# Optimization experiments

Measured on AMD Instinct MI355X. Metric: run time of the kernel, lower is better.

## Reference

```python
import jax, jax.numpy as jnp
import numpy as np

EPS_IN = 1e-5   # InstanceNorm2d default eps
EPS_VAR = 1e-6  # clamp on attention variance

def instance_norm(x):
    # x: (b, c, h, w); affine=False, biased variance over spatial dims
    mean = jnp.mean(x, axis=(2, 3), keepdims=True)
    var = jnp.var(x, axis=(2, 3), keepdims=True)
    return (x - mean) * jax.lax.rsqrt(var + EPS_IN)

def setup_inputs() -> dict:
    key = jax.random.key(0)
    k1, k2, k3, k4 = jax.random.split(key, 4)
    shp = (4, 512, 64, 64)
    return {
        "c_x": jax.random.normal(k1, shp, dtype=jnp.float32),
        "s_x": jax.random.normal(k2, shp, dtype=jnp.float32),
        "c_1x": jax.random.normal(k3, shp, dtype=jnp.float32),
        "s_1x": jax.random.normal(k4, shp, dtype=jnp.float32),
    }

def reference(c_x, s_x, c_1x, s_1x):
    b, v_dim, h, w = c_x.shape
    hw = h * w
    # Q: (b, hw, qk), K: (b, qk, hw), V: (b, hw, v)
    Q = instance_norm(c_1x).reshape(b, -1, hw).transpose(0, 2, 1)
    K = instance_norm(s_1x).reshape(b, -1, s_1x.shape[2] * s_1x.shape[3])
    V = s_x.reshape(b, v_dim, -1).transpose(0, 2, 1)
    # attention over spatial tokens
    A = jax.nn.softmax(jnp.einsum('bqc,bck->bqk', Q, K), axis=-1)
    M = jnp.einsum('bqk,bkv->bqv', A, V)              # weighted mean
    Var = jnp.einsum('bqk,bkv->bqv', A, V * V) - M * M  # weighted variance
    S = jnp.sqrt(jnp.clip(Var, EPS_VAR, None))
    # back to (b, v, h, w)
    M = M.reshape(b, h, w, -1).transpose(0, 3, 1, 2)
    S = S.reshape(b, h, w, -1).transpose(0, 3, 1, 2)
    return S * instance_norm(c_x) + M
```

## Files before the change

### kernel.cpp

```cpp
#include <hip/hip_runtime.h>
#include <cmath>


#define B_  4
#define C_  512
#define HW_ 4096

typedef _Float16 f16;
typedef _Float16 f16x8 __attribute__((ext_vector_type(8)));
typedef float    f32x4 __attribute__((ext_vector_type(4)));

__device__ __forceinline__ f32x4 mfma16(f16x8 a, f16x8 b, f32x4 c) {
  return __builtin_amdgcn_mfma_f32_16x16x32_f16(a, b, c, 0, 0, 0);
}
__device__ __forceinline__ void g2l16(const f16* g, f16* l) {
  __builtin_amdgcn_global_load_lds(
      (const __attribute__((address_space(1))) void*)g,
      (__attribute__((address_space(3))) void*)l, 16, 0, 0);
}

__global__ __launch_bounds__(256) void k_stats(
    const float* __restrict__ cx, const float* __restrict__ c1,
    const float* __restrict__ s1,
    float2* __restrict__ cxs, float2* __restrict__ c1s, float2* __restrict__ s1s) {
  int c = blockIdx.x, b = blockIdx.y, t = blockIdx.z;
  const float* src = (t == 0 ? cx : (t == 1 ? c1 : s1)) + (size_t)(b * C_ + c) * HW_;
  float s = 0.f, q = 0.f;
  const float4* src4 = (const float4*)src;
  for (int i = threadIdx.x; i < HW_ / 4; i += 256) {
    float4 v = src4[i];
    s += v.x + v.y + v.z + v.w;
    q += v.x * v.x + v.y * v.y + v.z * v.z + v.w * v.w;
  }
#pragma unroll
  for (int off = 1; off < 64; off <<= 1) {
    s += __shfl_xor(s, off);
    q += __shfl_xor(q, off);
  }
  __shared__ float ss[4], sq[4];
  int wv = threadIdx.x >> 6;
  if ((threadIdx.x & 63) == 0) { ss[wv] = s; sq[wv] = q; }
  __syncthreads();
  if (threadIdx.x == 0) {
    float S = ss[0] + ss[1] + ss[2] + ss[3];
    float Q = sq[0] + sq[1] + sq[2] + sq[3];
    float mean = S * (1.f / HW_);
    float var = Q * (1.f / HW_) - mean * mean;
    float2 r;
    r.x = mean;
    r.y = rsqrtf(var + 1e-5f);
    (t == 0 ? cxs : (t == 1 ? c1s : s1s))[b * C_ + c] = r;
  }
}

__global__ __launch_bounds__(256) void k_prept(
    const float* __restrict__ src, const float2* __restrict__ st,
    f16* __restrict__ dst) {
  int pb = blockIdx.x * 64, cb = blockIdx.y * 64, b = blockIdx.z;
  __shared__ float t[64][65];
  int tj = threadIdx.x & 63, tr = threadIdx.x >> 6;
#pragma unroll 4
  for (int p = 0; p < 16; ++p) {
    int cl = p * 4 + tr;
    float2 mr = st[b * C_ + cb + cl];
    float v = src[(size_t)(b * C_ + cb + cl) * HW_ + pb + tj];
    t[cl][tj] = (v - mr.x) * mr.y;
  }
  __syncthreads();
#pragma unroll 4
  for (int p = 0; p < 16; ++p) {
    int pr = p * 4 + tr;
    dst[(size_t)(b * HW_ + pb + pr) * C_ + cb + tj] = (f16)t[tj][pr];
  }
}

__global__ __launch_bounds__(256) void k_prepv(const float* __restrict__ src,
                                               f16* __restrict__ dst) {
  int gid = blockIdx.x * 256 + threadIdx.x;
  const float4* s = (const float4*)src + (size_t)gid * 2;
  float4 v0 = s[0], v1 = s[1];
  f16x8 v = {(f16)v0.x, (f16)v0.y, (f16)v0.z, (f16)v0.w,
             (f16)v1.x, (f16)v1.y, (f16)v1.z, (f16)v1.w};
  *(f16x8*)(dst + (size_t)gid * 8) = v;
}

__global__ __launch_bounds__(512, 2) void k_qk(
    const f16* __restrict__ Qt, const f16* __restrict__ Kt,
    f16* __restrict__ E, float2* __restrict__ mlpart,
    int qspan, int qt256, int npair) {
  int id = blockIdx.x, pair, kt;
  if ((npair & 7) == 0) {
    int xcd = id & 7, j = id >> 3, qrs = npair >> 3;
    pair = xcd * qrs + (j % qrs);
    kt = j / qrs;
  } else {
    pair = id >> 4;
    kt = id & 15;
  }
  int bz = pair / qt256, qt = pair - bz * qt256;

  const f16* Aq = Qt + ((size_t)(bz * qspan + qt * 256)) * C_;
  const f16* Bk = Kt + (size_t)bz * HW_ * C_ + (size_t)kt * 256 * C_;
  f16* Eb = E + ((size_t)(bz * qspan + qt * 256)) * HW_ + kt * 256;
  float2* mlb = mlpart + ((size_t)(bz * qspan + qt * 256)) * 16 + kt;

  __shared__ __align__(16) union ShQK {
    f16 ring[2 * 32768];
    f16 ebuf[64 * 272];
  } sh;
  __shared__ float sred[2][256];

  int t = threadIdx.x, wave = t >> 6, lane = t & 63, lq = lane & 15, quad = lane >> 4;
  int wy = wave >> 1, wx = wave & 1;

  int srow = t >> 3;
  int scol = ((t & 7) ^ (srow & 7)) * 8;

  int aoff = (wy * 64 + lq) * 64;
  int boff = 16384 + (wx * 128 + lq) * 64;
  int cx0 = (quad * 8) ^ ((lq & 7) << 3);
  int cx1 = (32 + quad * 8) ^ ((lq & 7) << 3);

  f32x4 acc[4][8];
#pragma unroll
  for (int mt = 0; mt < 4; ++mt)
#pragma unroll
    for (int nt = 0; nt < 8; ++nt) acc[mt][nt] = (f32x4){0, 0, 0, 0};

#pragma unroll
  for (int i = 0; i < 4; ++i)
    g2l16(Aq + (size_t)(i * 64 + srow) * C_ + scol, sh.ring + i * 4096 + t * 8);
#pragma unroll
  for (int i = 0; i < 4; ++i)
    g2l16(Bk + (size_t)(i * 64 + srow) * C_ + scol, sh.ring + 16384 + i * 4096 + t * 8);
  asm volatile("s_waitcnt vmcnt(0)" ::: "memory");
  __builtin_amdgcn_s_barrier();

  int cur = 0;
  for (int s = 0; s < 8; ++s) {
    const f16* base = sh.ring + cur * 32768;
    int nxOff = (cur ^ 1) * 32768;
    bool st = s < 7;
    int c1g = (s + 1) * 64;

    f16x8 af[4], bf[8];
#pragma unroll
    for (int mt = 0; mt < 4; ++mt)
      af[mt] = *(const f16x8*)(base + aoff + mt * 1024 + cx0);
#pragma unroll
    for (int nt = 0; nt < 8; ++nt)
      bf[nt] = *(const f16x8*)(base + boff + nt * 1024 + cx0);
    if (st) {
#pragma unroll
      for (int i = 0; i < 4; ++i)
        g2l16(Aq + (size_t)(i * 64 + srow) * C_ + c1g + scol,
              sh.ring + nxOff + i * 4096 + t * 8);
    }
    asm volatile("s_waitcnt lgkmcnt(0)" ::: "memory");
    __builtin_amdgcn_sched_barrier(0);
    __builtin_amdgcn_s_setprio(1);
#pragma unroll
    for (int mt = 0; mt < 4; ++mt)
#pragma unroll
      for (int nt = 0; nt < 8; ++nt)
        acc[mt][nt] = mfma16(af[mt], bf[nt], acc[mt][nt]);
    __builtin_amdgcn_s_setprio(0);

#pragma unroll
    for (int mt = 0; mt < 4; ++mt)
      af[mt] = *(const f16x8*)(base + aoff + mt * 1024 + cx1);
#pragma unroll
    for (int nt = 0; nt < 8; ++nt)
      bf[nt] = *(const f16x8*)(base + boff + nt * 1024 + cx1);
    if (st) {
#pragma unroll
      for (int i = 0; i < 4; ++i)
        g2l16(Bk + (size_t)(i * 64 + srow) * C_ + c1g + scol,
              sh.ring + nxOff + 16384 + i * 4096 + t * 8);
    }
    asm volatile("s_waitcnt lgkmcnt(0)" ::: "memory");
    __builtin_amdgcn_sched_barrier(0);
    __builtin_amdgcn_s_setprio(1);
#pragma unroll
    for (int mt = 0; mt < 4; ++mt)
#pragma unroll
      for (int nt = 0; nt < 8; ++nt)
        acc[mt][nt] = mfma16(af[mt], bf[nt], acc[mt][nt]);
    __builtin_amdgcn_s_setprio(0);

    asm volatile("s_waitcnt vmcnt(0)" ::: "memory");
    __builtin_amdgcn_s_barrier();
    cur ^= 1;
  }

#pragma unroll
  for (int mt = 0; mt < 4; ++mt)
#pragma unroll
    for (int r = 0; r < 4; ++r) {
      float v = -1e30f;
#pragma unroll
      for (int nt = 0; nt < 8; ++nt) v = fmaxf(v, acc[mt][nt][r]);
#pragma unroll
      for (int msk = 1; msk < 16; msk <<= 1) v = fmaxf(v, __shfl_xor(v, msk));
      if (lq == 0) sred[wx][wy * 64 + mt * 16 + quad * 4 + r] = v;
    }
  __syncthreads();
  float mrow[4][4];
#pragma unroll
  for (int mt = 0; mt < 4; ++mt)
#pragma unroll
    for (int r = 0; r < 4; ++r) {
      int rr = wy * 64 + mt * 16 + quad * 4 + r;
      mrow[mt][r] = fmaxf(sred[0][rr], sred[1][rr]);
    }

  float rsum[4][4];
#pragma unroll
  for (int mt = 0; mt < 4; ++mt)
#pragma unroll
    for (int r = 0; r < 4; ++r) rsum[mt][r] = 0.f;

#pragma unroll
  for (int mt = 0; mt < 4; ++mt) {
    __syncthreads();
#pragma unroll
    for (int nt = 0; nt < 8; ++nt) {
      f32x4 v = acc[mt][nt];
      int cs = ((wx * 16 + nt * 2 + (lq >> 3)) ^ (quad << 1)) * 8 + (lq & 7);
#pragma unroll
      for (int r = 0; r < 4; ++r) {
        float e = __expf(v[r] - mrow[mt][r]);
        rsum[mt][r] += e;
        sh.ebuf[(wy * 16 + quad * 4 + r) * 272 + cs] = (f16)e;
      }
    }
    __syncthreads();
#pragma unroll
    for (int i = 0; i < 4; ++i) {
      int idx = i * 512 + t;
      int rl = idx >> 5, ck = idx & 31;
      int cr = (ck ^ (((rl >> 2) & 3) << 1)) * 8;
      f16x8 v8 = *(const f16x8*)(sh.ebuf + rl * 272 + cr);
      int grow = (rl >> 4) * 64 + mt * 16 + (rl & 15);
      *(f16x8*)(Eb + (size_t)grow * HW_ + ck * 8) = v8;
    }
  }

#pragma unroll
  for (int mt = 0; mt < 4; ++mt)
#pragma unroll
    for (int r = 0; r < 4; ++r) {
      float v = rsum[mt][r];
#pragma unroll
      for (int msk = 1; msk < 16; msk <<= 1) v += __shfl_xor(v, msk);
      if (lq == 0) sred[wx][wy * 64 + mt * 16 + quad * 4 + r] = v;
    }
  __syncthreads();
  if (wx == 0 && lq == 0) {
#pragma unroll
    for (int mt = 0; mt < 4; ++mt)
#pragma unroll
      for (int r = 0; r < 4; ++r) {
        int rr = wy * 64 + mt * 16 + quad * 4 + r;
        mlb[(size_t)rr * 16] = make_float2(mrow[mt][r], sred[0][rr] + sred[1][rr]);
      }
  }
}

__global__ __launch_bounds__(256) void k_red(const float2* __restrict__ mlpart,
                                             float* __restrict__ alpha) {
  int row = blockIdx.x * 256 + threadIdx.x;
  const float2* p = mlpart + (size_t)row * 16;
  float2 loc[16];
  float m = -1e30f;
#pragma unroll
  for (int i = 0; i < 16; ++i) {
    loc[i] = p[i];
    m = fmaxf(m, loc[i].x);
  }
  float l = 0.f;
#pragma unroll
  for (int i = 0; i < 16; ++i) l += loc[i].y * __expf(loc[i].x - m);
  float invl = 1.f / l;
#pragma unroll
  for (int i = 0; i < 16; ++i)
    alpha[(size_t)row * 16 + i] = __expf(loc[i].x - m) * invl;
}

#define PV_STAGE_A(i)                                                         \
  g2l16(Ap + (size_t)((i)*64 + srow) * HW_ + s2 * 64 + scol,                  \
        sm + pnOff + (i)*4096 + t * 8)
#define PV_STAGE_B(i)                                                         \
  g2l16(Bv + (size_t)((i)*64 + srow) * HW_ + s2 * 64 + scol,                  \
        sm + pnOff + 16384 + (i)*4096 + t * 8)

#define PV_PHASE(CX, STAGE_STMT, POST_STMT)                                   \
  {                                                                           \
    f16x8 af0 = *(const f16x8*)(As_s + aoff + 0 * 1024 + (CX));               \
    f16x8 af1 = *(const f16x8*)(As_s + aoff + 1 * 1024 + (CX));               \
    f16x8 af2 = *(const f16x8*)(As_s + aoff + 2 * 1024 + (CX));               \
    f16x8 af3 = *(const f16x8*)(As_s + aoff + 3 * 1024 + (CX));               \
    f16x8 bf0 = *(const f16x8*)(Bs_s + boff + 0 * 1024 + (CX));               \
    f16x8 bf1 = *(const f16x8*)(Bs_s + boff + 1 * 1024 + (CX));               \
    f16x8 bf2 = *(const f16x8*)(Bs_s + boff + 2 * 1024 + (CX));               \
    f16x8 bf3 = *(const f16x8*)(Bs_s + boff + 3 * 1024 + (CX));               \
    STAGE_STMT;                                                               \
    asm volatile("s_waitcnt lgkmcnt(0)" ::: "memory");                        \
    __builtin_amdgcn_sched_barrier(0);                                        \
    __builtin_amdgcn_s_setprio(1);                                            \
    af0 *= aal[0]; af1 *= aal[1]; af2 *= aal[2]; af3 *= aal[3];               \
    f16x8 q0 = bf0 * bf0, q1 = bf1 * bf1, q2 = bf2 * bf2, q3 = bf3 * bf3;     \
    accM [0][0] = mfma16(af0, bf0, accM [0][0]);                              \
    accM2[0][0] = mfma16(af0, q0,  accM2[0][0]);                              \
    accM [0][1] = mfma16(af0, bf1, accM [0][1]);                              \
    accM2[0][1] = mfma16(af0, q1,  accM2[0][1]);                              \
    accM [0][2] = mfma16(af0, bf2, accM [0][2]);                              \
    accM2[0][2] = mfma16(af0, q2,  accM2[0][2]);                              \
    accM [0][3] = mfma16(af0, bf3, accM [0][3]);                              \
    accM2[0][3] = mfma16(af0, q3,  accM2[0][3]);                              \
    accM [1][0] = mfma16(af1, bf0, accM [1][0]);                              \
    accM2[1][0] = mfma16(af1, q0,  accM2[1][0]);                              \
    accM [1][1] = mfma16(af1, bf1, accM [1][1]);                              \
    accM2[1][1] = mfma16(af1, q1,  accM2[1][1]);                              \
    accM [1][2] = mfma16(af1, bf2, accM [1][2]);                              \
    accM2[1][2] = mfma16(af1, q2,  accM2[1][2]);                              \
    accM [1][3] = mfma16(af1, bf3, accM [1][3]);                              \
    accM2[1][3] = mfma16(af1, q3,  accM2[1][3]);                              \
    accM [2][0] = mfma16(af2, bf0, accM [2][0]);                              \
    accM2[2][0] = mfma16(af2, q0,  accM2[2][0]);                              \
    accM [2][1] = mfma16(af2, bf1, accM [2][1]);                              \
    accM2[2][1] = mfma16(af2, q1,  accM2[2][1]);                              \
    accM [2][2] = mfma16(af2, bf2, accM [2][2]);                              \
    accM2[2][2] = mfma16(af2, q2,  accM2[2][2]);                              \
    accM [2][3] = mfma16(af2, bf3, accM [2][3]);                              \
    accM2[2][3] = mfma16(af2, q3,  accM2[2][3]);                              \
    accM [3][0] = mfma16(af3, bf0, accM [3][0]);                              \
    accM2[3][0] = mfma16(af3, q0,  accM2[3][0]);                              \
    accM [3][1] = mfma16(af3, bf1, accM [3][1]);                              \
    accM2[3][1] = mfma16(af3, q1,  accM2[3][1]);                              \
    accM [3][2] = mfma16(af3, bf2, accM [3][2]);                              \
    accM2[3][2] = mfma16(af3, q2,  accM2[3][2]);                              \
    accM [3][3] = mfma16(af3, bf3, accM [3][3]);                              \
    accM2[3][3] = mfma16(af3, q3,  accM2[3][3]);                              \
    __builtin_amdgcn_s_setprio(0);                                            \
    POST_STMT;                                                                \
  }

__global__ __launch_bounds__(512, 2) void k_pv(
    const f16* __restrict__ P, const float* __restrict__ alphaG,
    const f16* __restrict__ V, const float* __restrict__ cx,
    const float2* __restrict__ cxs, float* __restrict__ out,
    int qspan, int qbase, int qt256) {
  int npairs = (int)gridDim.x >> 2;
  int id = blockIdx.x, pair, ct;
  if ((npairs & 7) == 0) {
    int x = id & 7, j = id >> 3, ppx = npairs >> 3;
    pair = x * ppx + (j >> 2);
    ct = j & 3;
  } else {
    pair = id >> 2;
    ct = id & 3;
  }
  int bz = pair / qt256, qt = pair - bz * qt256;

  const f16* Ap = P + ((size_t)(bz * qspan + qt * 256)) * HW_;
  const f16* Bv = V + ((size_t)(bz * C_ + ct * 128)) * HW_;

  __shared__ __align__(16) f16 sm[3 * 24576 + 256 * 17];
  f16* Alh = sm + 3 * 24576;

  int t = threadIdx.x, wave = t >> 6, lane = t & 63, lq = lane & 15, quad = lane >> 4;
  int wy = wave >> 1, wx = wave & 1;

  {
    const float* ag = alphaG + ((size_t)(bz * qspan + qt * 256)) * 16;
#pragma unroll
    for (int i = 0; i < 8; ++i) {
      int e = i * 512 + t;
      Alh[(e >> 4) * 17 + (e & 15)] = (f16)ag[e];
    }
  }

  int srow = t >> 3;
  int scol = ((t & 7) ^ (srow & 7)) * 8;

  int aoff = (wy * 64 + lq) * 64;
  int boff = (wx * 64 + lq) * 64;
  int cx0 = (quad * 8) ^ ((lq & 7) << 3);
  int cx1 = (32 + quad * 8) ^ ((lq & 7) << 3);

  f32x4 accM[4][4], accM2[4][4];
#pragma unroll
  for (int mt = 0; mt < 4; ++mt)
#pragma unroll
    for (int nt = 0; nt < 4; ++nt) {
      accM[mt][nt] = (f32x4){0, 0, 0, 0};
      accM2[mt][nt] = (f32x4){0, 0, 0, 0};
    }

#pragma unroll
  for (int s0 = 0; s0 < 2; ++s0) {
    int off = s0 * 24576;
#pragma unroll
    for (int i = 0; i < 4; ++i)
      g2l16(Ap + (size_t)(i * 64 + srow) * HW_ + s0 * 64 + scol,
            sm + off + i * 4096 + t * 8);
#pragma unroll
    for (int i = 0; i < 2; ++i)
      g2l16(Bv + (size_t)(i * 64 + srow) * HW_ + s0 * 64 + scol,
            sm + off + 16384 + i * 4096 + t * 8);
  }
  asm volatile("s_waitcnt lgkmcnt(0)" ::: "memory");
  asm volatile("s_waitcnt vmcnt(6)" ::: "memory");
  __builtin_amdgcn_s_barrier();

  int ph = 0, pn = 2;
  for (int s = 0; s < 64; ++s) {
    const f16* As_s = sm + ph * 24576;
    const f16* Bs_s = As_s + 16384;
    int pnOff = pn * 24576;
    int s2 = s + 2;
    bool st = s < 62;
    int ktl = s >> 2;
    f16 aal[4];
    aal[0] = Alh[(wy * 64 + lq +  0) * 17 + ktl];
    aal[1] = Alh[(wy * 64 + lq + 16) * 17 + ktl];
    aal[2] = Alh[(wy * 64 + lq + 32) * 17 + ktl];
    aal[3] = Alh[(wy * 64 + lq + 48) * 17 + ktl];

    PV_PHASE(cx0,
             if (st) { PV_STAGE_A(0); PV_STAGE_A(1); PV_STAGE_A(2); }, )
    PV_PHASE(cx1,
             if (st) { PV_STAGE_A(3); PV_STAGE_B(0); PV_STAGE_B(1); },
             if (st) { asm volatile("s_waitcnt vmcnt(6)" ::: "memory"); }
             else    { asm volatile("s_waitcnt vmcnt(0)" ::: "memory"); })
    __builtin_amdgcn_s_barrier();

    ph = (ph == 2) ? 0 : ph + 1;
    pn = (pn == 2) ? 0 : pn + 1;
  }

  int chbase = ct * 128 + wx * 64;
#pragma unroll
  for (int mt = 0; mt < 4; ++mt) {
    int q0 = qbase + qt * 256 + wy * 64 + mt * 16 + quad * 4;
#pragma unroll
    for (int nt = 0; nt < 4; ++nt) {
      int c = chbase + nt * 16 + lq;
      float2 stc = cxs[bz * C_ + c];
      size_t base = ((size_t)bz * C_ + c) * HW_ + q0;
      float4 cv = *(const float4*)(cx + base);
      f32x4 m1 = accM[mt][nt], m2 = accM2[mt][nt];
      float4 o;
      o.x = sqrtf(fmaxf(m2[0] - m1[0] * m1[0], 1e-6f)) * ((cv.x - stc.x) * stc.y) + m1[0];
      o.y = sqrtf(fmaxf(m2[1] - m1[1] * m1[1], 1e-6f)) * ((cv.y - stc.x) * stc.y) + m1[1];
      o.z = sqrtf(fmaxf(m2[2] - m1[2] * m1[2], 1e-6f)) * ((cv.z - stc.x) * stc.y) + m1[2];
      o.w = sqrtf(fmaxf(m2[3] - m1[3] * m1[3], 1e-6f)) * ((cv.w - stc.x) * stc.y) + m1[3];
      *(float4*)(out + base) = o;
    }
  }
}

extern "C" void kernel_launch(void* const* d_in, const int* in_sizes, int n_in,
                              void* d_out, int out_size, void* d_ws,
                              size_t ws_size, hipStream_t stream) {
  const float* c_x = (const float*)d_in[0];
  const float* s_x = (const float*)d_in[1];
  const float* c1x = (const float*)d_in[2];
  const float* s1x = (const float*)d_in[3];
  float* out = (float*)d_out;

  char* ws = (char*)d_ws;
  size_t o = 0;
  f16* Qt = (f16*)(ws + o);  o += (size_t)B_ * HW_ * C_ * 2;
  f16* Kt = (f16*)(ws + o);  o += (size_t)B_ * HW_ * C_ * 2;
  f16* Vh = (f16*)(ws + o);  o += (size_t)B_ * HW_ * C_ * 2;
  float2* cxs = (float2*)(ws + o); o += B_ * C_ * sizeof(float2);
  float2* c1s = (float2*)(ws + o); o += B_ * C_ * sizeof(float2);
  float2* s1s = (float2*)(ws + o); o += B_ * C_ * sizeof(float2);
  size_t fixed = (o + 255) & ~(size_t)255;

  const size_t per_row = (size_t)HW_ * 2 + 16 * 8 + 16 * 4;
  struct Cfg { int nb, qs; };
  const Cfg cfgs[5] = {{4, 4096}, {1, 4096}, {1, 2048}, {1, 1024}, {1, 512}};
  Cfg cfg = cfgs[4];
  for (int i = 0; i < 5; ++i) {
    size_t rows = (size_t)cfgs[i].nb * cfgs[i].qs;
    if (fixed + rows * per_row <= ws_size) { cfg = cfgs[i]; break; }
  }
  const int nb = cfg.nb, qspan = cfg.qs, qt256 = qspan / 256;
  const int npair256 = nb * qt256;
  const size_t rows = (size_t)nb * qspan;
  f16* E = (f16*)(ws + fixed);
  float2* mlpart = (float2*)(ws + fixed + rows * HW_ * 2);
  float* alpha = (float*)(ws + fixed + rows * HW_ * 2 + rows * 16 * 8);

  k_stats<<<dim3(C_, B_, 3), 256, 0, stream>>>(c_x, c1x, s1x, cxs, c1s, s1s);
  k_prept<<<dim3(HW_ / 64, C_ / 64, B_), 256, 0, stream>>>(c1x, c1s, Qt);
  k_prept<<<dim3(HW_ / 64, C_ / 64, B_), 256, 0, stream>>>(s1x, s1s, Kt);
  k_prepv<<<dim3(B_ * C_ * HW_ / 8 / 256), 256, 0, stream>>>(s_x, Vh);

  for (int b0 = 0; b0 < B_; b0 += nb) {
    for (int qb = 0; qb < HW_; qb += qspan) {
      const f16* Qtp = Qt + ((size_t)b0 * HW_ + qb) * C_;
      const f16* Ktp = Kt + (size_t)b0 * HW_ * C_;
      const f16* Vp = Vh + (size_t)b0 * C_ * HW_;
      const float* cxp = c_x + (size_t)b0 * C_ * HW_;
      const float2* cxsp = cxs + b0 * C_;
      float* outp = out + (size_t)b0 * C_ * HW_;

      k_qk<<<dim3((unsigned)(npair256 * 16)), 512, 0, stream>>>(
          Qtp, Ktp, E, mlpart, qspan, qt256, npair256);
      k_red<<<dim3((unsigned)(rows / 256)), 256, 0, stream>>>(mlpart, alpha);
      k_pv<<<dim3((unsigned)(npair256 * 4)), 512, 0, stream>>>(
          E, alpha, Vp, cxp, cxsp, outp, qspan, qb, qt256);
    }
  }
}
```

Baseline: 390.6 us.

## Shrink PV tile to 128x128 with 256 threads and double-buffered staging

Reworks k_pv from a 256-query by 128-channel tile with 512 threads and a three-stage LDS ring to a 128x128 tile with 256 threads and a simple two-buffer scheme. All eight global-to-LDS loads for the next K step are issued in the first phase, followed by a full vmcnt(0) wait and a barrier each iteration. The grid doubles in block count and LDS per block shrinks, aiming for better load balance and more resident blocks per CU. In exchange, each V tile is reused across fewer queries, and the shallower pipeline with a full memory wait every step gives less latency hiding.

Measured after the change: 387.1 us. Within noise of the previous version (-0.9%).

```diff
diff --git a/kernel.cpp b/kernel.cpp
--- a/kernel.cpp
+++ b/kernel.cpp
@@ -287,12 +287,17 @@
     alpha[(size_t)row * 16 + i] = __expf(loc[i].x - m) * invl;
 }
 
-#define PV_STAGE_A(i)                                                         \
-  g2l16(Ap + (size_t)((i)*64 + srow) * HW_ + s2 * 64 + scol,                  \
-        sm + pnOff + (i)*4096 + t * 8)
-#define PV_STAGE_B(i)                                                         \
-  g2l16(Bv + (size_t)((i)*64 + srow) * HW_ + s2 * 64 + scol,                  \
-        sm + pnOff + 16384 + (i)*4096 + t * 8)
+#define PV_STAGE_ALL8()                                                       \
+  {                                                                           \
+    _Pragma("unroll")                                                         \
+    for (int i = 0; i < 4; ++i)                                               \
+      g2l16(Ap + (size_t)(i * 32 + srow) * HW_ + s1g + scol,                  \
+            nx + i * 2048 + t * 8);                                           \
+    _Pragma("unroll")                                                         \
+    for (int i = 0; i < 4; ++i)                                               \
+      g2l16(Bv + (size_t)(i * 32 + srow) * HW_ + s1g + scol,                  \
+            nx + 8192 + i * 2048 + t * 8);                                    \
+  }
 
 #define PV_PHASE(CX, STAGE_STMT, POST_STMT)                                   \
   {                                                                           \
@@ -346,11 +351,11 @@
     POST_STMT;                                                                \
   }
 
-__global__ __launch_bounds__(512, 2) void k_pv(
+__global__ __launch_bounds__(256, 2) void k_pv(
     const f16* __restrict__ P, const float* __restrict__ alphaG,
     const f16* __restrict__ V, const float* __restrict__ cx,
     const float2* __restrict__ cxs, float* __restrict__ out,
-    int qspan, int qbase, int qt256) {
+    int qspan, int qbase, int qt128) {
   int npairs = (int)gridDim.x >> 2;
   int id = blockIdx.x, pair, ct;
   if ((npairs & 7) == 0) {
@@ -361,22 +366,22 @@
     pair = id >> 2;
     ct = id & 3;
   }
-  int bz = pair / qt256, qt = pair - bz * qt256;
-
-  const f16* Ap = P + ((size_t)(bz * qspan + qt * 256)) * HW_;
+  int bz = pair / qt128, qt = pair - bz * qt128;
+
+  const f16* Ap = P + ((size_t)(bz * qspan + qt * 128)) * HW_;
   const f16* Bv = V + ((size_t)(bz * C_ + ct * 128)) * HW_;
 
-  __shared__ __align__(16) f16 sm[3 * 24576 + 256 * 17];
-  f16* Alh = sm + 3 * 24576;
+  __shared__ __align__(16) f16 sm[2 * 16384 + 128 * 17];
+  f16* Alh = sm + 2 * 16384;
 
   int t = threadIdx.x, wave = t >> 6, lane = t & 63, lq = lane & 15, quad = lane >> 4;
   int wy = wave >> 1, wx = wave & 1;
 
   {
-    const float* ag = alphaG + ((size_t)(bz * qspan + qt * 256)) * 16;
+    const float* ag = alphaG + ((size_t)(bz * qspan + qt * 128)) * 16;
 #pragma unroll
     for (int i = 0; i < 8; ++i) {
-      int e = i * 512 + t;
+      int e = i * 256 + t;
       Alh[(e >> 4) * 17 + (e & 15)] = (f16)ag[e];
     }
   }
@@ -385,7 +390,7 @@
   int scol = ((t & 7) ^ (srow & 7)) * 8;
 
   int aoff = (wy * 64 + lq) * 64;
-  int boff = (wx * 64 + lq) * 64;
+  int boff = 8192 + (wx * 64 + lq) * 64;
   int cx0 = (quad * 8) ^ ((lq & 7) << 3);
   int cx1 = (32 + quad * 8) ^ ((lq & 7) << 3);
 
@@ -398,29 +403,22 @@
       accM2[mt][nt] = (f32x4){0, 0, 0, 0};
     }
 
-#pragma unroll
-  for (int s0 = 0; s0 < 2; ++s0) {
-    int off = s0 * 24576;
-#pragma unroll
-    for (int i = 0; i < 4; ++i)
-      g2l16(Ap + (size_t)(i * 64 + srow) * HW_ + s0 * 64 + scol,
-            sm + off + i * 4096 + t * 8);
-#pragma unroll
-    for (int i = 0; i < 2; ++i)
-      g2l16(Bv + (size_t)(i * 64 + srow) * HW_ + s0 * 64 + scol,
-            sm + off + 16384 + i * 4096 + t * 8);
+  {
+    f16* nx = sm;
+    int s1g = 0;
+    PV_STAGE_ALL8();
   }
   asm volatile("s_waitcnt lgkmcnt(0)" ::: "memory");
-  asm volatile("s_waitcnt vmcnt(6)" ::: "memory");
+  asm volatile("s_waitcnt vmcnt(0)" ::: "memory");
   __builtin_amdgcn_s_barrier();
 
-  int ph = 0, pn = 2;
+  int cur = 0;
   for (int s = 0; s < 64; ++s) {
-    const f16* As_s = sm + ph * 24576;
-    const f16* Bs_s = As_s + 16384;
-    int pnOff = pn * 24576;
-    int s2 = s + 2;
-    bool st = s < 62;
+    const f16* As_s = sm + cur * 16384;
+    const f16* Bs_s = As_s;
+    f16* nx = sm + (cur ^ 1) * 16384;
+    int s1g = (s + 1) * 64;
+    bool st = s < 63;
     int ktl = s >> 2;
     f16 aal[4];
     aal[0] = Alh[(wy * 64 + lq +  0) * 17 + ktl];
@@ -428,22 +426,17 @@
     aal[2] = Alh[(wy * 64 + lq + 32) * 17 + ktl];
     aal[3] = Alh[(wy * 64 + lq + 48) * 17 + ktl];
 
-    PV_PHASE(cx0,
-             if (st) { PV_STAGE_A(0); PV_STAGE_A(1); PV_STAGE_A(2); }, )
-    PV_PHASE(cx1,
-             if (st) { PV_STAGE_A(3); PV_STAGE_B(0); PV_STAGE_B(1); },
-             if (st) { asm volatile("s_waitcnt vmcnt(6)" ::: "memory"); }
-             else    { asm volatile("s_waitcnt vmcnt(0)" ::: "memory"); })
+    PV_PHASE(cx0, if (st) PV_STAGE_ALL8(), )
+    PV_PHASE(cx1, , )
+    asm volatile("s_waitcnt vmcnt(0)" ::: "memory");
     __builtin_amdgcn_s_barrier();
-
-    ph = (ph == 2) ? 0 : ph + 1;
-    pn = (pn == 2) ? 0 : pn + 1;
+    cur ^= 1;
   }
 
   int chbase = ct * 128 + wx * 64;
 #pragma unroll
   for (int mt = 0; mt < 4; ++mt) {
-    int q0 = qbase + qt * 256 + wy * 64 + mt * 16 + quad * 4;
+    int q0 = qbase + qt * 128 + wy * 64 + mt * 16 + quad * 4;
 #pragma unroll
     for (int nt = 0; nt < 4; ++nt) {
       int c = chbase + nt * 16 + lq;
@@ -488,8 +481,10 @@
     size_t rows = (size_t)cfgs[i].nb * cfgs[i].qs;
     if (fixed + rows * per_row <= ws_size) { cfg = cfgs[i]; break; }
   }
-  const int nb = cfg.nb, qspan = cfg.qs, qt256 = qspan / 256;
+  const int nb = cfg.nb, qspan = cfg.qs;
+  const int qt256 = qspan / 256, qt128 = qspan / 128;
   const int npair256 = nb * qt256;
+  const int npair128 = nb * qt128;
   const size_t rows = (size_t)nb * qspan;
   f16* E = (f16*)(ws + fixed);
   float2* mlpart = (float2*)(ws + fixed + rows * HW_ * 2);
@@ -512,8 +507,8 @@
       k_qk<<<dim3((unsigned)(npair256 * 16)), 512, 0, stream>>>(
           Qtp, Ktp, E, mlpart, qspan, qt256, npair256);
       k_red<<<dim3((unsigned)(rows / 256)), 256, 0, stream>>>(mlpart, alpha);
-      k_pv<<<dim3((unsigned)(npair256 * 4)), 512, 0, stream>>>(
-          E, alpha, Vp, cxp, cxsp, outp, qspan, qb, qt256);
-    }
-  }
-}
+      k_pv<<<dim3((unsigned)(npair128 * 4)), 256, 0, stream>>>(
+          E, alpha, Vp, cxp, cxsp, outp, qspan, qb, qt128);
+    }
+  }
+}
```
